# Kernel optimization log

Measured on AMD Instinct MI355X. Metric: run time of the kernel, lower is better.

## Reference

```python
import jax, jax.numpy as jnp
import numpy as np

# Asymmetric NF4 lookup table: NFQuantizer.create_normal_map(offset=0.9677083, num_bits=4)
NF4_TABLE = jnp.array([
    -1.0, -0.6961928009986877, -0.5250730514526367, -0.39491748809814453,
    -0.28444138169288635, -0.18477343022823334, -0.09105003625154495, 0.0,
    0.07958029955625534, 0.16093020141124725, 0.24611230194568634,
    0.33791524171829224, 0.44070982933044434, 0.5626170039176941,
    0.7229568362236023, 1.0], dtype=jnp.float32)

OUT_FEATURES = 4096
IN_FEATURES = 4096
BLOCK_SIZE = 64
NUM_BITS = 4

def setup_inputs() -> dict:
    key = jax.random.key(0)
    k1, k2, k3, k4, k5 = jax.random.split(key, 5)
    n_packed = OUT_FEATURES * IN_FEATURES // (8 // NUM_BITS)      # 8388608
    n_blocks = OUT_FEATURES * IN_FEATURES // BLOCK_SIZE            # 262144
    return {
        "input": jax.random.normal(k1, (2, 1024, IN_FEATURES), dtype=jnp.float32),
        "qweight": jax.random.randint(k2, (n_packed, 1), 0, 256, dtype=jnp.int32),
        "absmax": jax.random.uniform(k3, (n_blocks, 1), dtype=jnp.float32, minval=0.01, maxval=0.05),
        "lora_A": jax.random.normal(k4, (64, IN_FEATURES), dtype=jnp.float32) * 0.02,
        "lora_B": jax.random.normal(k5, (OUT_FEATURES, 64), dtype=jnp.float32) * 0.02,
    }

def dequantize_block(qweight, absmax):
    q = qweight[:, 0]                         # [N/2] packed bytes (int)
    low = NF4_TABLE[q & 0xF]                  # sub-code i=0 (low nibble first)
    high = NF4_TABLE[(q >> 4) & 0xF]          # sub-code i=1
    w = jnp.stack([low, high], axis=-1)       # [N/2, 2], matches torch column order
    w = w.reshape(-1, BLOCK_SIZE) * absmax    # per-block rescale, absmax [n_blocks,1]
    return w.reshape(OUT_FEATURES, IN_FEATURES)

def reference(input, qweight, absmax, lora_A, lora_B):
    weight = dequantize_block(qweight, absmax)          # [out, in] fp32
    ret = input @ weight.T                              # [B, S, out]
    lora = (input @ lora_A.T) @ lora_B.T                # low-rank path
    return ret + lora
```

## Files before the change

### kernel.cpp

```cpp
#include <hip/hip_runtime.h>
#include <hip/hip_bf16.h>
#include <stdint.h>

#define M_DIM 2048
#define N_DIM 4096
#define K_DIM 4096

typedef __attribute__((ext_vector_type(8))) __bf16 bf16x8;
typedef __attribute__((ext_vector_type(4))) float f32x4;
typedef __attribute__((ext_vector_type(8))) unsigned short u16x8;

__device__ __constant__ float NF4_TAB[16] = {
    -1.0f, -0.6961928009986877f, -0.5250730514526367f, -0.39491748809814453f,
    -0.28444138169288635f, -0.18477343022823334f, -0.09105003625154495f, 0.0f,
    0.07958029955625534f, 0.16093020141124725f, 0.24611230194568634f,
    0.33791524171829224f, 0.44070982933044434f, 0.5626170039176941f,
    0.7229568362236023f, 1.0f};

__device__ inline unsigned short f2b(float f) {
  union { float f; uint32_t u; } v; v.f = f;
  uint32_t u = v.u;
  return (unsigned short)((u + 0x7fffu + ((u >> 16) & 1u)) >> 16);
}

__global__ void k_cvt3(const float4* __restrict__ in, ushort4* __restrict__ A16,
                       const float4* __restrict__ lA, ushort4* __restrict__ lA16,
                       const float4* __restrict__ lB, ushort4* __restrict__ lB16) {
  int b = blockIdx.x;
  const float4* src;
  ushort4* dst;
  int i;
  if (b < 8192)      { src = in; dst = A16;  i = b * 256 + threadIdx.x; }
  else if (b < 8448) { src = lA; dst = lA16; i = (b - 8192) * 256 + threadIdx.x; }
  else               { src = lB; dst = lB16; i = (b - 8448) * 256 + threadIdx.x; }
  float4 v = src[i];
  ushort4 o;
  o.x = f2b(v.x); o.y = f2b(v.y); o.z = f2b(v.z); o.w = f2b(v.w);
  dst[i] = o;
}

__global__ void __launch_bounds__(256) k_build_w(const int* __restrict__ qw,
                                                 const float* __restrict__ am,
                                                 unsigned short* __restrict__ W) {
  __shared__ float tab[16];
  const int t = threadIdx.x;
  if (t < 16) tab[t] = NF4_TAB[t];
  __syncthreads();
  size_t i = (size_t)blockIdx.x * 256 + t;
  int4 q = *(const int4*)(qw + i * 4);
  float amv = am[i >> 3];
  u16x8 o;
  o[0] = f2b(tab[q.x & 15] * amv);  o[1] = f2b(tab[(q.x >> 4) & 15] * amv);
  o[2] = f2b(tab[q.y & 15] * amv);  o[3] = f2b(tab[(q.y >> 4) & 15] * amv);
  o[4] = f2b(tab[q.z & 15] * amv);  o[5] = f2b(tab[(q.z >> 4) & 15] * amv);
  o[6] = f2b(tab[q.w & 15] * amv);  o[7] = f2b(tab[(q.w >> 4) & 15] * amv);
  *(u16x8*)(W + i * 8) = o;
}

__global__ void __launch_bounds__(256) k_lora_u(const unsigned short* __restrict__ A16,
                                                const unsigned short* __restrict__ lA16,
                                                float* __restrict__ Up) {
  const int ln = threadIdx.x & 63, w = threadIdx.x >> 6;
  const int lr = ln & 15, lk = ln >> 4;
  const int mslab = blockIdx.x & 15;
  const int kc = blockIdx.x >> 4;
  const int m0 = mslab * 128 + w * 32;
  const int k0 = kc * 256;
  f32x4 acc[2][4] = {};
#pragma unroll
  for (int kk = 0; kk < 256; kk += 32) {
    bf16x8 af[2], bv[4];
#pragma unroll
    for (int mi = 0; mi < 2; ++mi)
      af[mi] = *(const bf16x8*)(A16 + (size_t)(m0 + mi * 16 + lr) * K_DIM + k0 + kk + lk * 8);
#pragma unroll
    for (int ni = 0; ni < 4; ++ni)
      bv[ni] = *(const bf16x8*)(lA16 + (size_t)(ni * 16 + lr) * K_DIM + k0 + kk + lk * 8);
#pragma unroll
    for (int mi = 0; mi < 2; ++mi)
#pragma unroll
      for (int ni = 0; ni < 4; ++ni)
        acc[mi][ni] = __builtin_amdgcn_mfma_f32_16x16x32_bf16(af[mi], bv[ni],
                                                              acc[mi][ni], 0, 0, 0);
  }
  float* up = Up + (size_t)kc * (M_DIM * 64);
#pragma unroll
  for (int mi = 0; mi < 2; ++mi)
#pragma unroll
    for (int ni = 0; ni < 4; ++ni)
#pragma unroll
      for (int r = 0; r < 4; ++r)
        up[(size_t)(m0 + mi * 16 + lk * 4 + r) * 64 + ni * 16 + lr] = acc[mi][ni][r];
}

__global__ void k_lora_red(const float4* __restrict__ Up, ushort4* __restrict__ U16) {
  int i = blockIdx.x * 256 + threadIdx.x;
  float4 s = Up[i];
#pragma unroll
  for (int c = 1; c < 16; ++c) {
    float4 p = Up[(size_t)c * (M_DIM * 64 / 4) + i];
    s.x += p.x; s.y += p.y; s.z += p.z; s.w += p.w;
  }
  ushort4 o; o.x = f2b(s.x); o.y = f2b(s.y); o.z = f2b(s.z); o.w = f2b(s.w);
  U16[i] = o;
}

#define LDSBUF 24576

#define FENCE() asm volatile("" ::: "memory")
#define BAR() do { FENCE(); __builtin_amdgcn_s_barrier(); FENCE(); } while (0)

#define READ_FRAGS(KS, BC, AF, BV)                                               \
  do {                                                                           \
    _Pragma("unroll") for (int mi = 0; mi < 4; ++mi) {                           \
      int row = wr * 64 + mi * 16 + lr;                                          \
      int slot = (((KS) << 2) | lk) ^ (row & 7);                                 \
      AF[mi] = *(const bf16x8*)((BC) + row * 64 + slot * 8);                     \
    }                                                                            \
    _Pragma("unroll") for (int ni = 0; ni < 4; ++ni) {                           \
      int row = wc * 64 + ni * 16 + lr;                                          \
      int slot = (((KS) << 2) | lk) ^ (row & 7);                                 \
      BV[ni] = *(const bf16x8*)((BC) + 8192 + row * 64 + slot * 8);              \
    }                                                                            \
  } while (0)

#define MFMA_CLUSTER(AF, BV)                                                     \
  do {                                                                           \
    __builtin_amdgcn_s_setprio(1);                                               \
    _Pragma("unroll") for (int mi = 0; mi < 4; ++mi)                             \
    _Pragma("unroll") for (int ni = 0; ni < 4; ++ni)                             \
      acc[mi][ni] = __builtin_amdgcn_mfma_f32_16x16x32_bf16(                     \
          AF[mi], BV[ni], acc[mi][ni], 0, 0, 0);                                 \
    __builtin_amdgcn_s_setprio(0);                                               \
  } while (0)

__global__ void __launch_bounds__(512, 2) k_gemm(const unsigned short* __restrict__ A,
                                                 const unsigned short* __restrict__ B,
                                                 const unsigned short* __restrict__ U,
                                                 const unsigned short* __restrict__ LB,
                                                 float* __restrict__ C) {
  __shared__ unsigned short lds[3 * LDSBUF];
  const int tid = threadIdx.x;
  const int ln = tid & 63;
  const int wid = tid >> 6;
  const int wr = wid >> 2;
  const int wc = wid & 3;
  const int lr = ln & 15;
  const int lk = ln >> 4;

  const int sw = (blockIdx.x & 7) * 32 + (blockIdx.x >> 3);
  const int bm = sw & 15;
  const int bn = sw >> 4;
  const size_t arow0 = (size_t)bm * 128;
  const size_t brow0 = (size_t)bn * 256;

  const int srow = (wid << 3) + (ln >> 3);
  const int gs0 = (ln & 7) ^ (srow & 7);
  auto stage = [&](const unsigned short* __restrict__ G, size_t stride, size_t grow0,
                   int kt, unsigned short* dst) {
    const char* g = (const char*)(G + (grow0 + srow) * stride) + kt * 128 + gs0 * 16;
    __builtin_amdgcn_global_load_lds(
        (const __attribute__((address_space(1))) uint32_t*)g,
        (__attribute__((address_space(3))) uint32_t*)(dst + (size_t)(wid << 3) * 64),
        16, 0, 0);
  };

  f32x4 acc[4][4] = {};

  stage(A, K_DIM, arow0, 0, lds);
  stage(A, K_DIM, arow0 + 64, 0, lds + 4096);
  stage(B, K_DIM, brow0, 0, lds + 8192);
  stage(B, K_DIM, brow0 + 64, 0, lds + 12288);
  stage(B, K_DIM, brow0 + 128, 0, lds + 16384);
  stage(B, K_DIM, brow0 + 192, 0, lds + 20480);
  {
    unsigned short* b1 = lds + LDSBUF;
    stage(A, K_DIM, arow0, 1, b1);
    stage(A, K_DIM, arow0 + 64, 1, b1 + 4096);
    stage(B, K_DIM, brow0, 1, b1 + 8192);
    stage(B, K_DIM, brow0 + 64, 1, b1 + 12288);
    stage(B, K_DIM, brow0 + 128, 1, b1 + 16384);
    stage(B, K_DIM, brow0 + 192, 1, b1 + 20480);
  }
  asm volatile("s_waitcnt vmcnt(6)" ::: "memory");
  BAR();

  int cb = 0, sb = 2;
#pragma unroll 1
  for (int t = 0; t < 65; ++t) {
    const unsigned short* bc = lds + cb * LDSBUF;
    unsigned short* sd = lds + sb * LDSBUF;
    int kt2 = t + 2;
    const bool lora = (kt2 >= 64);
    const unsigned short* GA = lora ? U : A;
    const unsigned short* GB = lora ? LB : B;
    const size_t str = lora ? 64 : (size_t)K_DIM;
    const int ktv = lora ? 0 : kt2;

    {
      bf16x8 af[4], bv[4];
      READ_FRAGS(0, bc, af, bv);
      stage(GA, str, arow0, ktv, sd);
      stage(GA, str, arow0 + 64, ktv, sd + 4096);
      stage(GB, str, brow0, ktv, sd + 8192);
      BAR();
      asm volatile("s_waitcnt lgkmcnt(0)" ::: "memory");
      __builtin_amdgcn_sched_barrier(0);
      MFMA_CLUSTER(af, bv);
      BAR();
    }

    {
      bf16x8 af[4], bv[4];
      READ_FRAGS(1, bc, af, bv);
      stage(GB, str, brow0 + 64, ktv, sd + 12288);
      stage(GB, str, brow0 + 128, ktv, sd + 16384);
      stage(GB, str, brow0 + 192, ktv, sd + 20480);
      asm volatile("s_waitcnt vmcnt(6)" ::: "memory");
      BAR();
      asm volatile("s_waitcnt lgkmcnt(0)" ::: "memory");
      __builtin_amdgcn_sched_barrier(0);
      MFMA_CLUSTER(af, bv);
      BAR();
    }

    cb = (cb == 2) ? 0 : cb + 1;
    sb = (sb == 2) ? 0 : sb + 1;
  }

  float* Cb = C + (arow0 + (size_t)wr * 64) * N_DIM + brow0 + wc * 64;
#pragma unroll
  for (int mi = 0; mi < 4; ++mi)
#pragma unroll
    for (int ni = 0; ni < 4; ++ni)
#pragma unroll
      for (int r = 0; r < 4; ++r)
        Cb[(size_t)(mi * 16 + lk * 4 + r) * N_DIM + ni * 16 + lr] = acc[mi][ni][r];
}

extern "C" void kernel_launch(void* const* d_in, const int* in_sizes, int n_in,
                              void* d_out, int out_size, void* d_ws, size_t ws_size,
                              hipStream_t stream) {
  const float* input  = (const float*)d_in[0];
  const int* qweight  = (const int*)d_in[1];
  const float* absmax = (const float*)d_in[2];
  const float* lora_A = (const float*)d_in[3];
  const float* lora_B = (const float*)d_in[4];
  float* out = (float*)d_out;

  unsigned short* A16  = (unsigned short*)d_ws;
  unsigned short* B16  = A16 + (size_t)M_DIM * K_DIM;
  unsigned short* lB16 = B16 + (size_t)N_DIM * K_DIM;
  unsigned short* lA16 = lB16 + (size_t)N_DIM * 64;
  unsigned short* U16  = lA16 + (size_t)64 * K_DIM;
  float* Up = (float*)B16;

  k_cvt3<<<8704, 256, 0, stream>>>((const float4*)input, (ushort4*)A16,
                                   (const float4*)lora_A, (ushort4*)lA16,
                                   (const float4*)lora_B, (ushort4*)lB16);
  k_lora_u<<<256, 256, 0, stream>>>(A16, lA16, Up);
  k_lora_red<<<(M_DIM * 64 / 4) / 256, 256, 0, stream>>>((const float4*)Up,
                                                         (ushort4*)U16);
  k_build_w<<<(N_DIM * K_DIM / 8) / 256, 256, 0, stream>>>(qweight, absmax, B16);
  k_gemm<<<256, 512, 0, stream>>>(A16, B16, U16, lB16, out);
}
```

Measured before the change: 104.3 us.

## Merge two half-k-step phases into one barrier per iteration

Restructures the main GEMM loop so all six tile loads are issued up front, both k-halves of fragments are read from LDS together, and all 32 MFMAs run in one cluster. The loop now has a single barrier per iteration instead of four, removing the explicit lgkmcnt waits and sched_barrier fences. This cuts synchronisation overhead but doubles fragment register pressure and leaves the interleaving of LDS reads and MFMAs to the compiler, which may hurt overlap at 2 blocks per CU.

```diff
diff --git a/kernel.cpp b/kernel.cpp
--- a/kernel.cpp
+++ b/kernel.cpp
@@ -110,30 +110,6 @@
 #define FENCE() asm volatile("" ::: "memory")
 #define BAR() do { FENCE(); __builtin_amdgcn_s_barrier(); FENCE(); } while (0)
 
-#define READ_FRAGS(KS, BC, AF, BV)                                               \
-  do {                                                                           \
-    _Pragma("unroll") for (int mi = 0; mi < 4; ++mi) {                           \
-      int row = wr * 64 + mi * 16 + lr;                                          \
-      int slot = (((KS) << 2) | lk) ^ (row & 7);                                 \
-      AF[mi] = *(const bf16x8*)((BC) + row * 64 + slot * 8);                     \
-    }                                                                            \
-    _Pragma("unroll") for (int ni = 0; ni < 4; ++ni) {                           \
-      int row = wc * 64 + ni * 16 + lr;                                          \
-      int slot = (((KS) << 2) | lk) ^ (row & 7);                                 \
-      BV[ni] = *(const bf16x8*)((BC) + 8192 + row * 64 + slot * 8);              \
-    }                                                                            \
-  } while (0)
-
-#define MFMA_CLUSTER(AF, BV)                                                     \
-  do {                                                                           \
-    __builtin_amdgcn_s_setprio(1);                                               \
-    _Pragma("unroll") for (int mi = 0; mi < 4; ++mi)                             \
-    _Pragma("unroll") for (int ni = 0; ni < 4; ++ni)                             \
-      acc[mi][ni] = __builtin_amdgcn_mfma_f32_16x16x32_bf16(                     \
-          AF[mi], BV[ni], acc[mi][ni], 0, 0, 0);                                 \
-    __builtin_amdgcn_s_setprio(0);                                               \
-  } while (0)
-
 __global__ void __launch_bounds__(512, 2) k_gemm(const unsigned short* __restrict__ A,
                                                  const unsigned short* __restrict__ B,
                                                  const unsigned short* __restrict__ U,
@@ -197,32 +173,48 @@
     const size_t str = lora ? 64 : (size_t)K_DIM;
     const int ktv = lora ? 0 : kt2;
 
-    {
-      bf16x8 af[4], bv[4];
-      READ_FRAGS(0, bc, af, bv);
-      stage(GA, str, arow0, ktv, sd);
-      stage(GA, str, arow0 + 64, ktv, sd + 4096);
-      stage(GB, str, brow0, ktv, sd + 8192);
-      BAR();
-      asm volatile("s_waitcnt lgkmcnt(0)" ::: "memory");
-      __builtin_amdgcn_sched_barrier(0);
-      MFMA_CLUSTER(af, bv);
-      BAR();
+    stage(GA, str, arow0, ktv, sd);
+    stage(GA, str, arow0 + 64, ktv, sd + 4096);
+    stage(GB, str, brow0, ktv, sd + 8192);
+    stage(GB, str, brow0 + 64, ktv, sd + 12288);
+    stage(GB, str, brow0 + 128, ktv, sd + 16384);
+    stage(GB, str, brow0 + 192, ktv, sd + 20480);
+
+    bf16x8 af[4][2], bv[4][2];
+#pragma unroll
+    for (int mi = 0; mi < 4; ++mi) {
+      int row = wr * 64 + mi * 16 + lr;
+      int rb = row * 64, x = row & 7;
+#pragma unroll
+      for (int ks = 0; ks < 2; ++ks) {
+        int slot = ((ks << 2) | lk) ^ x;
+        af[mi][ks] = *(const bf16x8*)(bc + rb + slot * 8);
+      }
     }
-
-    {
-      bf16x8 af[4], bv[4];
-      READ_FRAGS(1, bc, af, bv);
-      stage(GB, str, brow0 + 64, ktv, sd + 12288);
-      stage(GB, str, brow0 + 128, ktv, sd + 16384);
-      stage(GB, str, brow0 + 192, ktv, sd + 20480);
-      asm volatile("s_waitcnt vmcnt(6)" ::: "memory");
-      BAR();
-      asm volatile("s_waitcnt lgkmcnt(0)" ::: "memory");
-      __builtin_amdgcn_sched_barrier(0);
-      MFMA_CLUSTER(af, bv);
-      BAR();
+#pragma unroll
+    for (int ni = 0; ni < 4; ++ni) {
+      int row = wc * 64 + ni * 16 + lr;
+      int rb = 8192 + row * 64, x = row & 7;
+#pragma unroll
+      for (int ks = 0; ks < 2; ++ks) {
+        int slot = ((ks << 2) | lk) ^ x;
+        bv[ni][ks] = *(const bf16x8*)(bc + rb + slot * 8);
+      }
     }
+
+    __builtin_amdgcn_s_setprio(1);
+#pragma unroll
+    for (int ks = 0; ks < 2; ++ks)
+#pragma unroll
+      for (int mi = 0; mi < 4; ++mi)
+#pragma unroll
+        for (int ni = 0; ni < 4; ++ni)
+          acc[mi][ni] = __builtin_amdgcn_mfma_f32_16x16x32_bf16(
+              af[mi][ks], bv[ni][ks], acc[mi][ni], 0, 0, 0);
+    __builtin_amdgcn_s_setprio(0);
+
+    asm volatile("s_waitcnt vmcnt(6)" ::: "memory");
+    BAR();
 
     cb = (cb == 2) ? 0 : cb + 1;
     sb = (sb == 2) ? 0 : sb + 1;
```

Result: no change. 103.7 us (-0.6%).
